# Performance work log

Measured on AMD Instinct MI355X. Metric: run time of the kernel, lower is better.

## Reference

```python
import jax, jax.numpy as jnp
import numpy as np

INPUT_HASH_SIZE = 4_000_000
ZCH_SIZE = 400_000
EMB_DIM = 128
N_IDS = 1_000_000


def _remap(ids, mch_sorted):
    """MCH-style ID remapping: binary-search raw id in the sorted ZCH id table.
    Matched ids map to their slot index; unmatched ids map to the last
    (collision/overflow) slot zch_size - 1."""
    zch_size = mch_sorted.shape[0]
    pos = jnp.searchsorted(mch_sorted, ids)
    pos = jnp.clip(pos, 0, zch_size - 1)
    hit = mch_sorted[pos] == ids
    return jnp.where(hit, pos, zch_size - 1)


def setup_inputs() -> dict:
    key = jax.random.key(0)
    k0, k1, k2, k3, k4, k5 = jax.random.split(key, 6)
    ids_0 = jax.random.randint(k0, (N_IDS,), 0, INPUT_HASH_SIZE, dtype=jnp.int64)
    ids_1 = jax.random.randint(k1, (N_IDS,), 0, INPUT_HASH_SIZE, dtype=jnp.int64)
    mch_ids_0 = jnp.sort(jax.random.randint(k2, (ZCH_SIZE,), 0, INPUT_HASH_SIZE, dtype=jnp.int64))
    mch_ids_1 = jnp.sort(jax.random.randint(k3, (ZCH_SIZE,), 0, INPUT_HASH_SIZE, dtype=jnp.int64))
    emb_0 = jax.random.normal(k4, (ZCH_SIZE, EMB_DIM), dtype=jnp.float32)
    emb_1 = jax.random.normal(k5, (ZCH_SIZE, EMB_DIM), dtype=jnp.float32)
    return {"ids_0": ids_0, "ids_1": ids_1, "mch_ids_0": mch_ids_0,
            "mch_ids_1": mch_ids_1, "emb_0": emb_0, "emb_1": emb_1}


def reference(ids_0, ids_1, mch_ids_0, mch_ids_1, emb_0, emb_1):
    # managed-collision remap per feature
    remapped_0 = _remap(ids_0, mch_ids_0)  # [N]
    remapped_1 = _remap(ids_1, mch_ids_1)  # [N]
    # embedding gather per feature -> [N, D]
    v0 = jnp.take(emb_0, remapped_0, axis=0)
    v1 = jnp.take(emb_1, remapped_1, axis=0)
    # pred = cat along dim 0, loss = mean
    pred = jnp.concatenate([v0, v1], axis=0)  # [2N, D]
    loss = pred.mean()
    return loss, remapped_0, remapped_1
```

## Files before the change

### kernel.cpp

```cpp
#include <hip/hip_runtime.h>
#include <stdint.h>

#define N_IDS     1000000
#define ZCH       400000
#define EMB_DIM   128
#define TOTAL     (2 * N_IDS)
#define HASH_SZ   4000000
#define BLOCK     256
#define GRID      ((TOTAL + BLOCK - 1) / BLOCK)
#define OVF       (ZCH - 1)
#define NBASE     16384


__global__ __launch_bounds__(256) void init_lut_kernel(uint4* __restrict__ lut)
{
    int t = blockIdx.x * blockDim.x + threadIdx.x;
    if (t < (2 * HASH_SZ) / 16)
        lut[t] = make_uint4(0xFFFFFFFFu, 0xFFFFFFFFu, 0xFFFFFFFFu, 0xFFFFFFFFu);
}

__device__ __forceinline__ int lower_bound_dev(const int* __restrict__ a, int target)
{
    int lo = 0, hi = ZCH;
    while (lo < hi) {
        int mid = (lo + hi) >> 1;
        if (a[mid] < target) lo = mid + 1; else hi = mid;
    }
    return lo;
}

__global__ __launch_bounds__(256) void build_lut_kernel(
    const int* __restrict__ mch0, const int* __restrict__ mch1,
    unsigned char* __restrict__ lut0, unsigned char* __restrict__ lut1,
    int* __restrict__ base0, int* __restrict__ base1)
{
    int t = blockIdx.x * blockDim.x + threadIdx.x;
    if (t < 2 * ZCH) {
        const int feat = t >= ZCH;
        const int s    = feat ? (t - ZCH) : t;
        const int* __restrict__ mch = feat ? mch1 : mch0;
        const int v = mch[s];
        if (s == 0 || mch[s - 1] != v) {
            const int lo = lower_bound_dev(mch, v & ~255);
            (feat ? lut1 : lut0)[v] = (unsigned char)(s - lo);
        }
    } else {
        int u = t - 2 * ZCH;
        if (u < 2 * NBASE) {
            const int feat = u >= NBASE;
            const int b    = feat ? (u - NBASE) : u;
            const int* __restrict__ mch = feat ? mch1 : mch0;
            (feat ? base1 : base0)[b] = lower_bound_dev(mch, b << 8);
        }
    }
}

__global__ __launch_bounds__(BLOCK) void remap_loss_kernel(
    const int* __restrict__ ids0, const int* __restrict__ ids1,
    const float* __restrict__ emb0, const float* __restrict__ emb1,
    const unsigned char* __restrict__ lut0, const unsigned char* __restrict__ lut1,
    const int* __restrict__ base0, const int* __restrict__ base1,
    float* __restrict__ out,
    float* __restrict__ partials)
{
    const int gid  = blockIdx.x * BLOCK + threadIdx.x;
    const int lane = threadIdx.x & 63;
    const int wave = threadIdx.x >> 6;

    float accl = 0.0f;

    const bool active = (gid < TOTAL);
    if (active) {
        const int feat = gid >= N_IDS;
        const int i    = feat ? (gid - N_IDS) : gid;
        const int id   = (feat ? ids1 : ids0)[i];
        const float* __restrict__ emb = feat ? emb1 : emb0;

        const unsigned int w = (feat ? lut1 : lut0)[id];
        const int          b = (feat ? base1 : base0)[id >> 8];
        const int rem = (w == 0xFFu) ? OVF : (b + (int)w);

        out[1 + gid] = (float)rem;

        const unsigned long long ovf = __ballot(rem == OVF);
        const int novf = __popcll(ovf);
        if (novf) {
            const float2* __restrict__ row =
                (const float2*)(emb + (size_t)OVF * EMB_DIM);
            float2 v = row[lane];
            float s = v.x + v.y;
            #pragma unroll
            for (int o = 32; o > 0; o >>= 1)
                s += __shfl_xor(s, o, 64);
            if (lane == 0) accl += (float)novf * s;
        }

        const int half = lane >> 5;
        const int l32  = lane & 31;
        unsigned long long hits = ~ovf;
        #pragma unroll 1
        while (hits) {
            int j0 = __ffsll(hits) - 1;
            hits &= hits - 1;
            const bool dup = (hits == 0);
            int j1 = dup ? j0 : (__ffsll(hits) - 1);
            if (!dup) hits &= hits - 1;
            int r = __shfl(rem, half ? j1 : j0, 64);
            const float4* __restrict__ row =
                (const float4*)(emb + (size_t)r * EMB_DIM);
            float4 v = row[l32];
            float s4 = (v.x + v.y) + (v.z + v.w);
            accl += (half && dup) ? 0.0f : s4;
        }
    }

    #pragma unroll
    for (int o = 32; o > 0; o >>= 1)
        accl += __shfl_down(accl, o, 64);

    __shared__ float wsum[BLOCK / 64];
    if (lane == 0) wsum[wave] = accl;
    __syncthreads();
    if (threadIdx.x == 0) {
        float s = 0.0f;
        #pragma unroll
        for (int w = 0; w < BLOCK / 64; ++w) s += wsum[w];
        partials[blockIdx.x] = s;
    }
}

__global__ __launch_bounds__(256) void finalize_kernel(
    const float* __restrict__ partials, float* __restrict__ out)
{
    __shared__ double sh[256];
    double s = 0.0;
    for (int i = threadIdx.x; i < GRID; i += 256)
        s += (double)partials[i];
    sh[threadIdx.x] = s;
    __syncthreads();
    #pragma unroll
    for (int stride = 128; stride > 0; stride >>= 1) {
        if (threadIdx.x < stride) sh[threadIdx.x] += sh[threadIdx.x + stride];
        __syncthreads();
    }
    if (threadIdx.x == 0)
        out[0] = (float)(sh[0] / ((double)TOTAL * (double)EMB_DIM));
}

extern "C" void kernel_launch(void* const* d_in, const int* in_sizes, int n_in,
                              void* d_out, int out_size, void* d_ws, size_t ws_size,
                              hipStream_t stream) {
    const int*   ids0 = (const int*)d_in[0];
    const int*   ids1 = (const int*)d_in[1];
    const int*   mch0 = (const int*)d_in[2];
    const int*   mch1 = (const int*)d_in[3];
    const float* emb0 = (const float*)d_in[4];
    const float* emb1 = (const float*)d_in[5];

    float* out = (float*)d_out;
    unsigned char* lut0 = (unsigned char*)d_ws;
    unsigned char* lut1 = lut0 + HASH_SZ;
    int*   base0    = (int*)(lut1 + HASH_SZ);
    int*   base1    = base0 + NBASE;
    float* partials = (float*)(base1 + NBASE);

    init_lut_kernel<<<((2 * HASH_SZ / 16) + 255) / 256, 256, 0, stream>>>(
        (uint4*)d_ws);
    build_lut_kernel<<<(2 * ZCH + 2 * NBASE + 255) / 256, 256, 0, stream>>>(
        mch0, mch1, lut0, lut1, base0, base1);
    remap_loss_kernel<<<GRID, BLOCK, 0, stream>>>(
        ids0, ids1, emb0, emb1, lut0, lut1, base0, base1, out, partials);
    finalize_kernel<<<1, 256, 0, stream>>>(partials, out);
}
```

Measured before the change: 389.0 us.

## Fuse LUT init and build into one chunked pass; fold finalize into last block

Replaces the separate LUT fill and scatter-build kernels with one kernel in which each thread owns a 16-entry chunk of the lookup table. The thread binary-searches its 256-bucket start, scans the sorted table entries that fall in its chunk, and writes the chunk as two 64-bit words. The final reduction kernel is removed: the last block of the remap kernel, found through an atomic counter, sums the partials. This cuts two launches and the separate memset pass, at the cost of 500k binary searches plus short linear scans instead of 400k.

After: 729.7 us. +87.6%, slower.

```diff
diff --git a/kernel.cpp b/kernel.cpp
--- a/kernel.cpp
+++ b/kernel.cpp
@@ -10,49 +10,55 @@
 #define GRID      ((TOTAL + BLOCK - 1) / BLOCK)
 #define OVF       (ZCH - 1)
 #define NBASE     16384
+#define NCHUNK    (HASH_SZ / 16)
 
 
-__global__ __launch_bounds__(256) void init_lut_kernel(uint4* __restrict__ lut)
+__global__ __launch_bounds__(256) void build_kernel(
+    const int* __restrict__ mch0, const int* __restrict__ mch1,
+    unsigned char* __restrict__ lut0, unsigned char* __restrict__ lut1,
+    int* __restrict__ base0, int* __restrict__ base1,
+    unsigned int* __restrict__ counter)
 {
-    int t = blockIdx.x * blockDim.x + threadIdx.x;
-    if (t < (2 * HASH_SZ) / 16)
-        lut[t] = make_uint4(0xFFFFFFFFu, 0xFFFFFFFFu, 0xFFFFFFFFu, 0xFFFFFFFFu);
-}
+    const int t = blockIdx.x * 256 + threadIdx.x;
+    if (t == 0) *counter = 0u;
+    if (t >= 2 * NCHUNK) return;
 
-__device__ __forceinline__ int lower_bound_dev(const int* __restrict__ a, int target)
-{
+    const int feat  = t >= NCHUNK;
+    const int c     = feat ? (t - NCHUNK) : t;
+    const int* __restrict__ mch = feat ? mch1 : mch0;
+
+    const int vbase  = c << 4;
+    const int bstart = vbase & ~255;
+
     int lo = 0, hi = ZCH;
     while (lo < hi) {
         int mid = (lo + hi) >> 1;
-        if (a[mid] < target) lo = mid + 1; else hi = mid;
+        if (mch[mid] < bstart) lo = mid + 1; else hi = mid;
     }
-    return lo;
-}
+    if ((c & 15) == 0) (feat ? base1 : base0)[c >> 4] = lo;
 
-__global__ __launch_bounds__(256) void build_lut_kernel(
-    const int* __restrict__ mch0, const int* __restrict__ mch1,
-    unsigned char* __restrict__ lut0, unsigned char* __restrict__ lut1,
-    int* __restrict__ base0, int* __restrict__ base1)
-{
-    int t = blockIdx.x * blockDim.x + threadIdx.x;
-    if (t < 2 * ZCH) {
-        const int feat = t >= ZCH;
-        const int s    = feat ? (t - ZCH) : t;
-        const int* __restrict__ mch = feat ? mch1 : mch0;
+    unsigned long long w0 = ~0ull, w1 = ~0ull;
+    const int vend = vbase + 16;
+    int s = lo;
+    int prev = (lo > 0) ? mch[lo - 1] : -1;
+    while (s < ZCH) {
         const int v = mch[s];
-        if (s == 0 || mch[s - 1] != v) {
-            const int lo = lower_bound_dev(mch, v & ~255);
-            (feat ? lut1 : lut0)[v] = (unsigned char)(s - lo);
+        if (v >= vend) break;
+        if (v >= vbase && v != prev) {
+            const unsigned long long d = (unsigned long long)(s - lo);
+            const int p = v - vbase;
+            if (p < 8) { const int sh = p * 8;
+                w0 = (w0 & ~(0xFFull << sh)) | (d << sh); }
+            else       { const int sh = (p - 8) * 8;
+                w1 = (w1 & ~(0xFFull << sh)) | (d << sh); }
         }
-    } else {
-        int u = t - 2 * ZCH;
-        if (u < 2 * NBASE) {
-            const int feat = u >= NBASE;
-            const int b    = feat ? (u - NBASE) : u;
-            const int* __restrict__ mch = feat ? mch1 : mch0;
-            (feat ? base1 : base0)[b] = lower_bound_dev(mch, b << 8);
-        }
+        prev = v;
+        ++s;
     }
+    unsigned long long* dst =
+        (unsigned long long*)((feat ? lut1 : lut0) + vbase);
+    dst[0] = w0;
+    dst[1] = w1;
 }
 
 __global__ __launch_bounds__(BLOCK) void remap_loss_kernel(
@@ -61,7 +67,8 @@
     const unsigned char* __restrict__ lut0, const unsigned char* __restrict__ lut1,
     const int* __restrict__ base0, const int* __restrict__ base1,
     float* __restrict__ out,
-    float* __restrict__ partials)
+    float* __restrict__ partials,
+    unsigned int* __restrict__ counter)
 {
     const int gid  = blockIdx.x * BLOCK + threadIdx.x;
     const int lane = threadIdx.x & 63;
@@ -127,24 +134,29 @@
         for (int w = 0; w < BLOCK / 64; ++w) s += wsum[w];
         partials[blockIdx.x] = s;
     }
-}
 
-__global__ __launch_bounds__(256) void finalize_kernel(
-    const float* __restrict__ partials, float* __restrict__ out)
-{
-    __shared__ double sh[256];
-    double s = 0.0;
-    for (int i = threadIdx.x; i < GRID; i += 256)
-        s += (double)partials[i];
-    sh[threadIdx.x] = s;
+    __shared__ bool amLast;
+    if (threadIdx.x == 0) {
+        __threadfence();
+        amLast = (atomicAdd(counter, 1u) == (unsigned)(GRID - 1));
+    }
     __syncthreads();
-    #pragma unroll
-    for (int stride = 128; stride > 0; stride >>= 1) {
-        if (threadIdx.x < stride) sh[threadIdx.x] += sh[threadIdx.x + stride];
+    if (amLast) {
+        __threadfence();
+        __shared__ double sh[BLOCK];
+        double sd = 0.0;
+        for (int i = threadIdx.x; i < GRID; i += BLOCK)
+            sd += (double)partials[i];
+        sh[threadIdx.x] = sd;
         __syncthreads();
+        #pragma unroll
+        for (int stride = BLOCK / 2; stride > 0; stride >>= 1) {
+            if (threadIdx.x < stride) sh[threadIdx.x] += sh[threadIdx.x + stride];
+            __syncthreads();
+        }
+        if (threadIdx.x == 0)
+            out[0] = (float)(sh[0] / ((double)TOTAL * (double)EMB_DIM));
     }
-    if (threadIdx.x == 0)
-        out[0] = (float)(sh[0] / ((double)TOTAL * (double)EMB_DIM));
 }
 
 extern "C" void kernel_launch(void* const* d_in, const int* in_sizes, int n_in,
@@ -163,12 +175,10 @@
     int*   base0    = (int*)(lut1 + HASH_SZ);
     int*   base1    = base0 + NBASE;
     float* partials = (float*)(base1 + NBASE);
+    unsigned int* counter = (unsigned int*)(partials + GRID);
 
-    init_lut_kernel<<<((2 * HASH_SZ / 16) + 255) / 256, 256, 0, stream>>>(
-        (uint4*)d_ws);
-    build_lut_kernel<<<(2 * ZCH + 2 * NBASE + 255) / 256, 256, 0, stream>>>(
-        mch0, mch1, lut0, lut1, base0, base1);
+    build_kernel<<<(2 * NCHUNK + 255) / 256, 256, 0, stream>>>(
+        mch0, mch1, lut0, lut1, base0, base1, counter);
     remap_loss_kernel<<<GRID, BLOCK, 0, stream>>>(
-        ids0, ids1, emb0, emb1, lut0, lut1, base0, base1, out, partials);
-    finalize_kernel<<<1, 256, 0, stream>>>(partials, out);
+        ids0, ids1, emb0, emb1, lut0, lut1, base0, base1, out, partials, counter);
 }
```
